# Performance work log

Hardware: AMD Instinct MI355X
Metric: run time of the kernel (lower is better)

## Reference

```python
import jax, jax.numpy as jnp
import numpy as np

N_DATA = 8192
M_QUERIES = 8192

def setup_inputs() -> dict:
    key = jax.random.key(0)
    k1, k2 = jax.random.split(key)
    data = jax.random.uniform(k1, (N_DATA, 3), dtype=jnp.float32)
    queries = jax.random.uniform(k2, (M_QUERIES, 3), dtype=jnp.float32)
    return {"data": data, "queries": queries, "radius": 0.1}

def reference(data, queries, radius):
    """Faithful jax version of native_neighbor_search.

    Returns (neighbors_index, neighbors_row_splits).
    Because jax.jit requires static shapes, neighbors_index is padded to the
    maximal size m*n with -1; the number of valid entries is
    neighbors_row_splits[-1]. Valid entries appear in the same row-major
    (query-ordered) order as torch's nonzero().
    """
    n = data.shape[0]
    m = queries.shape[0]
    # pairwise Euclidean distances [m, n] via the ||q||^2 + ||d||^2 - 2 q.d expansion
    q2 = jnp.sum(queries * queries, axis=1, keepdims=True)          # [m,1]
    d2 = jnp.sum(data * data, axis=1, keepdims=True).T              # [1,n]
    dists = jnp.sqrt(jnp.maximum(q2 + d2 - 2.0 * (queries @ data.T), 0.0))
    mask = dists <= radius                                          # [m,n]
    # CSR row splits: exclusive prefix sum of per-query neighbor counts
    counts = jnp.sum(mask.astype(jnp.int32), axis=1)                # [m]
    row_splits = jnp.concatenate(
        [jnp.zeros((1,), jnp.int32), jnp.cumsum(counts)])           # [m+1]
    # flattened nonzero in row-major order -> column index = flat % n
    (flat_idx,) = jnp.nonzero(mask.ravel(), size=m * n, fill_value=-1)
    neighbors_index = jnp.where(flat_idx >= 0, flat_idx % n, -1).astype(jnp.int32)
    return neighbors_index, row_splits
```

## Files before the change

### kernel.cpp

```cpp
#include <hip/hip_runtime.h>
#include <stdint.h>


#define N8 8192
#define C0 2097152
#define C04 (C0 / 4)
#define SLAB 524288
#define N4TOT ((size_t)N8 * N8 / 4)

__device__ __forceinline__ float next_up(float x) {
    return __uint_as_float(__float_as_uint(x) + 1u);
}
__device__ __forceinline__ float next_down(float x) {
    return __uint_as_float(__float_as_uint(x) - 1u);
}

__device__ __forceinline__ float sq_threshold(float r) {
    float T = __fmul_rn(r, r);
    while (__fsqrt_rn(T) > r) T = next_down(T);
    while (__fsqrt_rn(next_up(T)) <= r) T = next_up(T);
    return T;
}

__device__ __forceinline__ float pair_metric(float qx, float qy, float qz, float q2,
                                             float dx, float dy, float dz) {
    float d2 = __fadd_rn(__fadd_rn(__fmul_rn(dx, dx), __fmul_rn(dy, dy)),
                         __fmul_rn(dz, dz));
    float dot = __builtin_fmaf(qz, dz, __builtin_fmaf(qy, dy, __fmul_rn(qx, dx)));
    return __fsub_rn(__fadd_rn(q2, d2), __fmul_rn(2.0f, dot));
}

__device__ __forceinline__ float bc_lane(float x, int j) {
    return __int_as_float(__builtin_amdgcn_readlane(__float_as_int(x), j));
}


__global__ __launch_bounds__(256) void fused_interleave(
    const float* __restrict__ data, const float* __restrict__ queries,
    const float* __restrict__ radius_p, int* __restrict__ out_idx,
    unsigned long long* __restrict__ masks, int* __restrict__ counts) {
    int bid = blockIdx.x;
    int tid = threadIdx.x;
    int lane = tid & 63;
    int wv = tid >> 6;
    int u = bid * 4 + wv;
    int c = u >> 6;
    int g = u & 63;

    float T = sq_threshold(radius_p[0]);

    int p = c * 64 + lane;
    float dx = data[3 * p + 0], dy = data[3 * p + 1], dz = data[3 * p + 2];
    float d2 = __fadd_rn(__fadd_rn(__fmul_rn(dx, dx), __fmul_rn(dy, dy)),
                         __fmul_rn(dz, dz));

    int q0 = g * 128 + lane, q1 = g * 128 + 64 + lane;
    float qx0 = queries[3 * q0 + 0], qy0 = queries[3 * q0 + 1],
          qz0 = queries[3 * q0 + 2];
    float q20 = __fadd_rn(__fadd_rn(__fmul_rn(qx0, qx0), __fmul_rn(qy0, qy0)),
                          __fmul_rn(qz0, qz0));
    float qx1 = queries[3 * q1 + 0], qy1 = queries[3 * q1 + 1],
          qz1 = queries[3 * q1 + 2];
    float q21 = __fadd_rn(__fadd_rn(__fmul_rn(qx1, qx1), __fmul_rn(qy1, qy1)),
                          __fmul_rn(qz1, qz1));

    unsigned long long mask0 = 0, mask1 = 0;

    int4* out4 = (int4*)out_idx;
    const int4 vm1 = make_int4(-1, -1, -1, -1);
    size_t fb = (size_t)C04 + (size_t)bid * 256 + tid;

#pragma unroll
    for (int j = 0; j < 64; ++j) {
        if ((j & 3) == 0)
            out4[fb + (size_t)(j >> 2) * SLAB] = vm1;
        float Px = bc_lane(dx, j), Py = bc_lane(dy, j);
        float Pz = bc_lane(dz, j), Pd2 = bc_lane(d2, j);
        float dot = __builtin_fmaf(qz0, Pz,
                      __builtin_fmaf(qy0, Py, __fmul_rn(qx0, Px)));
        float uu = __fsub_rn(__fadd_rn(q20, Pd2), __fmul_rn(2.0f, dot));
        if (uu <= T) mask0 |= (1ull << j);
    }
#pragma unroll
    for (int j = 0; j < 64; ++j) {
        if ((j & 3) == 0 && j < 60)
            out4[fb + (size_t)(16 + (j >> 2)) * SLAB] = vm1;
        float Px = bc_lane(dx, j), Py = bc_lane(dy, j);
        float Pz = bc_lane(dz, j), Pd2 = bc_lane(d2, j);
        float dot = __builtin_fmaf(qz1, Pz,
                      __builtin_fmaf(qy1, Py, __fmul_rn(qx1, Px)));
        float uu = __fsub_rn(__fadd_rn(q21, Pd2), __fmul_rn(2.0f, dot));
        if (uu <= T) mask1 |= (1ull << j);
    }

    masks[(size_t)q0 * 128 + c] = mask0;
    masks[(size_t)q1 * 128 + c] = mask1;
    atomicAdd(&counts[q0], __popcll(mask0));
    atomicAdd(&counts[q1], __popcll(mask1));
}

__global__ __launch_bounds__(256) void scanemit_fill_tail(
    const unsigned long long* __restrict__ masks, const int* __restrict__ counts,
    int* __restrict__ out_idx, int* __restrict__ rs) {
    __shared__ int part[256];
    __shared__ int s_cnt[32];
    __shared__ int s_base[4];
    int b = blockIdx.x;
    int t = threadIdx.x;
    int wave = t >> 6;
    int lane = t & 63;

    int s = 0;
#pragma unroll 8
    for (int k = 0; k < 32; ++k) s += counts[t * 32 + k];
    part[t] = s;
    __syncthreads();
    for (int off = 1; off < 256; off <<= 1) {
        int v = 0;
        if (t >= off) v = part[t - off];
        __syncthreads();
        if (t >= off) part[t] += v;
        __syncthreads();
    }
    int c32 = b >> 3;
    if (t < 32) s_cnt[t] = counts[c32 * 32 + t];
    __syncthreads();
    if (t < 4) {
        int q = b * 4 + t;
        int excl = (c32 == 0) ? 0 : part[c32 - 1];
        int o = q & 31;
        int sum = 0;
        for (int k = 0; k < o; ++k) sum += s_cnt[k];
        int v = excl + sum;
        s_base[t] = v;
        rs[q] = v;
    }
    if (b == 2047 && t == 0) rs[N8] = part[255];
    __syncthreads();
    int L = part[255];

    {
        int q = b * 4 + wave;
        unsigned long long lo = masks[(size_t)q * 128 + lane];
        unsigned long long hi = masks[(size_t)q * 128 + 64 + lane];
        int plo = __popcll(lo), phi = __popcll(hi);
        int ilo = plo, ihi = phi;
        for (int off = 1; off < 64; off <<= 1) {
            int a = __shfl_up(ilo, off, 64);
            int bsh = __shfl_up(ihi, off, 64);
            if (lane >= off) { ilo += a; ihi += bsh; }
        }
        int total_lo = __shfl(ilo, 63, 64);
        int base = s_base[wave];
        int pos_lo = base + ilo - plo;
        int pos_hi = base + total_lo + ihi - phi;
        int jb_lo = lane * 64, jb_hi = (64 + lane) * 64;
        while (lo) {
            int bt = __builtin_ctzll(lo);
            out_idx[pos_lo++] = jb_lo + bt;
            lo &= lo - 1;
        }
        while (hi) {
            int bt = __builtin_ctzll(hi);
            out_idx[pos_hi++] = jb_hi + bt;
            hi &= hi - 1;
        }
    }

    int Lr = (L + 3) & ~3;
    if (b == 0 && t < (Lr - L)) out_idx[L + t] = -1;
    int4* out4 = (int4*)out_idx;
    const int4 v = make_int4(-1, -1, -1, -1);
    int i = (Lr >> 2) + b * 256 + t;
    const int stride = 2048 * 256;
    for (; i < C04; i += stride) out4[i] = v;
}


__global__ __launch_bounds__(256) void fill_kernel(int* __restrict__ out, size_t total) {
    size_t n4 = total >> 2;
    int4* out4 = (int4*)out;
    size_t i = (size_t)blockIdx.x * blockDim.x + threadIdx.x;
    size_t stride = (size_t)gridDim.x * blockDim.x;
    const int4 v = make_int4(-1, -1, -1, -1);
    for (; i < n4; i += stride) out4[i] = v;
    if (blockIdx.x == 0 && threadIdx.x == 0) {
        for (size_t k = n4 << 2; k < total; ++k) out[k] = -1;
    }
}

__global__ __launch_bounds__(256) void count_kernel(
    const float* __restrict__ data, const float* __restrict__ queries,
    const float* __restrict__ radius_p, int n, int m, int* __restrict__ counts) {
    int q = (blockIdx.x * blockDim.x + threadIdx.x) >> 6;
    int lane = threadIdx.x & 63;
    if (q >= m) return;
    float r = radius_p[0];
    float T = sq_threshold(r);
    float qx = queries[3 * q + 0], qy = queries[3 * q + 1], qz = queries[3 * q + 2];
    float q2 = __fadd_rn(__fadd_rn(__fmul_rn(qx, qx), __fmul_rn(qy, qy)),
                         __fmul_rn(qz, qz));
    int cnt = 0;
    for (int j = lane; j < n; j += 64) {
        float u = pair_metric(qx, qy, qz, q2, data[3 * j], data[3 * j + 1], data[3 * j + 2]);
        if (u <= T) cnt++;
    }
    for (int off = 32; off > 0; off >>= 1) cnt += __shfl_down(cnt, off, 64);
    if (lane == 0) counts[q] = cnt;
}

__global__ __launch_bounds__(1024) void scan_kernel2(const int* __restrict__ counts,
                                                     int* __restrict__ rs, int m) {
    __shared__ int part[1024];
    int t = threadIdx.x;
    int base = t * 8;
    int c[8];
    int s = 0;
    for (int k = 0; k < 8; ++k) {
        int p = base + k;
        c[k] = (p < m) ? counts[p] : 0;
        s += c[k];
    }
    part[t] = s;
    __syncthreads();
    for (int off = 1; off < 1024; off <<= 1) {
        int v = 0;
        if (t >= off) v = part[t - off];
        __syncthreads();
        if (t >= off) part[t] += v;
        __syncthreads();
    }
    int run = (t == 0) ? 0 : part[t - 1];
    for (int k = 0; k < 8; ++k) {
        int p = base + k;
        if (p < m) rs[p] = run;
        run += c[k];
    }
    if (t == 1023) rs[m] = part[1023];
}

__global__ __launch_bounds__(256) void emit_kernel(
    const float* __restrict__ data, const float* __restrict__ queries,
    const float* __restrict__ radius_p, int n, int m,
    const int* __restrict__ row_splits, int* __restrict__ out_idx) {
    int q = (blockIdx.x * blockDim.x + threadIdx.x) >> 6;
    int lane = threadIdx.x & 63;
    if (q >= m) return;
    float r = radius_p[0];
    float T = sq_threshold(r);
    float qx = queries[3 * q + 0], qy = queries[3 * q + 1], qz = queries[3 * q + 2];
    float q2 = __fadd_rn(__fadd_rn(__fmul_rn(qx, qx), __fmul_rn(qy, qy)),
                         __fmul_rn(qz, qz));
    int base = row_splits[q];
    unsigned long long lane_mask_lt = (lane == 0) ? 0ULL : (~0ULL >> (64 - lane));
    for (int j0 = 0; j0 < n; j0 += 64) {
        int j = j0 + lane;
        bool pred = false;
        if (j < n) {
            float u = pair_metric(qx, qy, qz, q2, data[3 * j], data[3 * j + 1], data[3 * j + 2]);
            pred = (u <= T);
        }
        unsigned long long mask = __ballot(pred);
        if (pred) {
            int pos = base + __popcll(mask & lane_mask_lt);
            out_idx[pos] = j;
        }
        base += __popcll(mask);
    }
}


extern "C" void kernel_launch(void* const* d_in, const int* in_sizes, int n_in,
                              void* d_out, int out_size, void* d_ws, size_t ws_size,
                              hipStream_t stream) {
    const float* data = (const float*)d_in[0];
    const float* queries = (const float*)d_in[1];
    const float* radius = (const float*)d_in[2];
    int n = in_sizes[0] / 3;
    int m = in_sizes[1] / 3;
    int* out = (int*)d_out;
    size_t idx_count = (size_t)m * (size_t)n;
    int* row = out + idx_count;

    size_t mask_bytes = (size_t)N8 * 128 * 8;
    size_t need = mask_bytes + N8 * 4;
    bool fast = (n == N8) && (m == N8) && (ws_size >= need);

    if (fast) {
        unsigned long long* masks = (unsigned long long*)d_ws;
        int* counts = (int*)((char*)d_ws + mask_bytes);
        hipMemsetAsync(counts, 0, N8 * sizeof(int), stream);
        fused_interleave<<<2048, 256, 0, stream>>>(data, queries, radius, out,
                                                   masks, counts);
        scanemit_fill_tail<<<2048, 256, 0, stream>>>(masks, counts, out, row);
    } else {
        fill_kernel<<<2048, 256, 0, stream>>>(out, idx_count);
        int blocks = (m * 64 + 255) / 256;
        count_kernel<<<blocks, 256, 0, stream>>>(data, queries, radius, n, m, row);
        scan_kernel2<<<1, 1024, 0, stream>>>(row, row, m);
        emit_kernel<<<blocks, 256, 0, stream>>>(data, queries, radius, n, m, row, out);
    }
}
```

Measured before the change: 72.31 us.

## Transpose mask layout and emit neighbors with one thread per query

Masks are now stored chunk-major (c*N8+q) so consecutive queries are contiguous. The emit stage changes from one wave per query with shuffle scans to one thread per query that walks all 128 mask words serially, and only the first 32 blocks do this work. This drops the per-wave prefix scans, but it concentrates emission in far fewer threads, each running long serial loops with scattered output writes. That risks a long tail in the second kernel.

```diff
diff --git a/kernel.cpp b/kernel.cpp
--- a/kernel.cpp
+++ b/kernel.cpp
@@ -38,7 +38,7 @@
 __global__ __launch_bounds__(256) void fused_interleave(
     const float* __restrict__ data, const float* __restrict__ queries,
     const float* __restrict__ radius_p, int* __restrict__ out_idx,
-    unsigned long long* __restrict__ masks, int* __restrict__ counts) {
+    unsigned long long* __restrict__ masks2, int* __restrict__ counts) {
     int bid = blockIdx.x;
     int tid = threadIdx.x;
     int lane = tid & 63;
@@ -93,22 +93,20 @@
         if (uu <= T) mask1 |= (1ull << j);
     }
 
-    masks[(size_t)q0 * 128 + c] = mask0;
-    masks[(size_t)q1 * 128 + c] = mask1;
+    masks2[(size_t)c * N8 + q0] = mask0;
+    masks2[(size_t)c * N8 + q1] = mask1;
     atomicAdd(&counts[q0], __popcll(mask0));
     atomicAdd(&counts[q1], __popcll(mask1));
 }
 
 __global__ __launch_bounds__(256) void scanemit_fill_tail(
-    const unsigned long long* __restrict__ masks, const int* __restrict__ counts,
+    const unsigned long long* __restrict__ masks2, const int* __restrict__ counts,
     int* __restrict__ out_idx, int* __restrict__ rs) {
     __shared__ int part[256];
     __shared__ int s_cnt[32];
-    __shared__ int s_base[4];
+    __shared__ int cnt256[256];
     int b = blockIdx.x;
     int t = threadIdx.x;
-    int wave = t >> 6;
-    int lane = t & 63;
 
     int s = 0;
 #pragma unroll 8
@@ -122,6 +120,7 @@
         if (t >= off) part[t] += v;
         __syncthreads();
     }
+
     int c32 = b >> 3;
     if (t < 32) s_cnt[t] = counts[c32 * 32 + t];
     __syncthreads();
@@ -131,39 +130,28 @@
         int o = q & 31;
         int sum = 0;
         for (int k = 0; k < o; ++k) sum += s_cnt[k];
-        int v = excl + sum;
-        s_base[t] = v;
-        rs[q] = v;
+        rs[q] = excl + sum;
     }
     if (b == 2047 && t == 0) rs[N8] = part[255];
-    __syncthreads();
     int L = part[255];
 
-    {
-        int q = b * 4 + wave;
-        unsigned long long lo = masks[(size_t)q * 128 + lane];
-        unsigned long long hi = masks[(size_t)q * 128 + 64 + lane];
-        int plo = __popcll(lo), phi = __popcll(hi);
-        int ilo = plo, ihi = phi;
-        for (int off = 1; off < 64; off <<= 1) {
-            int a = __shfl_up(ilo, off, 64);
-            int bsh = __shfl_up(ihi, off, 64);
-            if (lane >= off) { ilo += a; ihi += bsh; }
-        }
-        int total_lo = __shfl(ilo, 63, 64);
-        int base = s_base[wave];
-        int pos_lo = base + ilo - plo;
-        int pos_hi = base + total_lo + ihi - phi;
-        int jb_lo = lane * 64, jb_hi = (64 + lane) * 64;
-        while (lo) {
-            int bt = __builtin_ctzll(lo);
-            out_idx[pos_lo++] = jb_lo + bt;
-            lo &= lo - 1;
-        }
-        while (hi) {
-            int bt = __builtin_ctzll(hi);
-            out_idx[pos_hi++] = jb_hi + bt;
-            hi &= hi - 1;
+    if (b < 32) {
+        cnt256[t] = counts[b * 256 + t];
+        __syncthreads();
+        int q = b * 256 + t;
+        int cq = q >> 5;
+        int base = (cq == 0) ? 0 : part[cq - 1];
+        int lo = t & ~31;
+        for (int k = lo; k < t; ++k) base += cnt256[k];
+        int pos = base;
+        for (int c = 0; c < 128; ++c) {
+            unsigned long long mk = masks2[(size_t)c * N8 + q];
+            int jb = c * 64;
+            while (mk) {
+                int bt = __builtin_ctzll(mk);
+                out_idx[pos++] = jb + bt;
+                mk &= mk - 1;
+            }
         }
     }
 
@@ -287,12 +275,12 @@
     bool fast = (n == N8) && (m == N8) && (ws_size >= need);
 
     if (fast) {
-        unsigned long long* masks = (unsigned long long*)d_ws;
+        unsigned long long* masks2 = (unsigned long long*)d_ws;
         int* counts = (int*)((char*)d_ws + mask_bytes);
-        hipMemsetAsync(counts, 0, N8 * sizeof(int), stream);
+        (void)hipMemsetAsync(counts, 0, N8 * sizeof(int), stream);
         fused_interleave<<<2048, 256, 0, stream>>>(data, queries, radius, out,
-                                                   masks, counts);
-        scanemit_fill_tail<<<2048, 256, 0, stream>>>(masks, counts, out, row);
+                                                   masks2, counts);
+        scanemit_fill_tail<<<2048, 256, 0, stream>>>(masks2, counts, out, row);
     } else {
         fill_kernel<<<2048, 256, 0, stream>>>(out, idx_count);
         int blocks = (m * 64 + 255) / 256;
```

Result: slower. 115.1 us (+59.1%).

## Aggregate per-block masks in LDS for coalesced writes and fewer atomics

Applied to the files above, without the earlier changes.

Blocks grow to 512 threads, so each block now covers 8 data chunks for the same 128 queries. Per-wave masks are staged in shared memory and written out as 16-byte vectors covering contiguous mask columns, instead of scattered 8-byte stores. Per-query counts are popcount-summed across the 8 chunks before a single atomicAdd, which cuts atomic traffic eightfold. The cost is a block barrier and LDS use. The -1 fill offsets are adjusted for the new block size.

```diff
diff --git a/kernel.cpp b/kernel.cpp
--- a/kernel.cpp
+++ b/kernel.cpp
@@ -35,17 +35,18 @@
 }
 
 
-__global__ __launch_bounds__(256) void fused_interleave(
+__global__ __launch_bounds__(512) void fused_interleave(
     const float* __restrict__ data, const float* __restrict__ queries,
     const float* __restrict__ radius_p, int* __restrict__ out_idx,
     unsigned long long* __restrict__ masks, int* __restrict__ counts) {
+    __shared__ unsigned long long mask_lds[128][8];
     int bid = blockIdx.x;
     int tid = threadIdx.x;
     int lane = tid & 63;
     int wv = tid >> 6;
-    int u = bid * 4 + wv;
-    int c = u >> 6;
-    int g = u & 63;
+    int cb = bid >> 6;
+    int g = bid & 63;
+    int c = cb * 8 + wv;
 
     float T = sq_threshold(radius_p[0]);
 
@@ -68,7 +69,7 @@
 
     int4* out4 = (int4*)out_idx;
     const int4 vm1 = make_int4(-1, -1, -1, -1);
-    size_t fb = (size_t)C04 + (size_t)bid * 256 + tid;
+    size_t fb = (size_t)C04 + (size_t)bid * 512 + tid;
 
 #pragma unroll
     for (int j = 0; j < 64; ++j) {
@@ -93,10 +94,27 @@
         if (uu <= T) mask1 |= (1ull << j);
     }
 
-    masks[(size_t)q0 * 128 + c] = mask0;
-    masks[(size_t)q1 * 128 + c] = mask1;
-    atomicAdd(&counts[q0], __popcll(mask0));
-    atomicAdd(&counts[q1], __popcll(mask1));
+    mask_lds[lane][wv] = mask0;
+    mask_lds[64 + lane][wv] = mask1;
+    __syncthreads();
+
+    {
+        int q_local = tid >> 2;
+        int quarter = tid & 3;
+        unsigned long long m0 = mask_lds[q_local][quarter * 2];
+        unsigned long long m1 = mask_lds[q_local][quarter * 2 + 1];
+        size_t base = (size_t)(g * 128 + q_local) * 128 + cb * 8 + quarter * 2;
+        ulonglong2 vv;
+        vv.x = m0;
+        vv.y = m1;
+        *(ulonglong2*)&masks[base] = vv;
+    }
+    if (tid < 128) {
+        int cnt = 0;
+#pragma unroll
+        for (int k = 0; k < 8; ++k) cnt += __popcll(mask_lds[tid][k]);
+        atomicAdd(&counts[g * 128 + tid], cnt);
+    }
 }
 
 __global__ __launch_bounds__(256) void scanemit_fill_tail(
@@ -289,8 +307,8 @@
     if (fast) {
         unsigned long long* masks = (unsigned long long*)d_ws;
         int* counts = (int*)((char*)d_ws + mask_bytes);
-        hipMemsetAsync(counts, 0, N8 * sizeof(int), stream);
-        fused_interleave<<<2048, 256, 0, stream>>>(data, queries, radius, out,
+        (void)hipMemsetAsync(counts, 0, N8 * sizeof(int), stream);
+        fused_interleave<<<1024, 512, 0, stream>>>(data, queries, radius, out,
                                                    masks, counts);
         scanemit_fill_tail<<<2048, 256, 0, stream>>>(masks, counts, out, row);
     } else {
```

Result: faster. 67.35 us (-6.8%).
